# Performance work log

Measured on AMD Instinct MI355X. Metric: run time of the kernel, lower is better.

Reference implementation:

```python
import jax, jax.numpy as jnp
import numpy as np

B, S, H = 2, 1024, 4096
NH, NKV, HD = 32, 8, 128
GROUPS = NH // NKV  # num_key_value_groups
ROPE_THETA = 10000.0


def setup_inputs() -> dict:
    key = jax.random.key(0)
    k0, k1, k2 = jax.random.split(key, 3)
    x = jax.random.normal(k0, (B, S, H), jnp.float32)
    w_qkv = jax.random.normal(k1, (H, (NH + 2 * NKV) * HD), jnp.float32) * (1.0 / np.sqrt(H))
    w_o = jax.random.normal(k2, (NH * HD, H), jnp.float32) * (1.0 / np.sqrt(H))
    # rotary cos/sin tables (llama freqs_cis, interleaved-pair convention)
    inv_freq = 1.0 / (ROPE_THETA ** (np.arange(0, HD, 2, dtype=np.float64) / HD))
    freqs = np.outer(np.arange(S, dtype=np.float64), inv_freq)  # [S, HD/2]
    cos = jnp.asarray(np.cos(freqs), jnp.float32)
    sin = jnp.asarray(np.sin(freqs), jnp.float32)
    # additive causal mask [1,1,S,S]
    causal = np.tril(np.ones((S, S), dtype=bool))
    mask = jnp.asarray(np.where(causal, 0.0, -1e9), jnp.float32)[None, None]
    return {"x": x, "w_qkv": w_qkv, "w_o": w_o, "cos": cos, "sin": sin, "mask": mask}


def _rope(t, cos, sin):
    # t: [B,S,N,HD]; rotate interleaved (even, odd) pairs like complex mult by freqs_cis
    t2 = t.reshape(t.shape[:-1] + (HD // 2, 2))
    t0, t1 = t2[..., 0], t2[..., 1]
    c = cos[None, :, None, :]  # [1,S,1,HD/2]
    s = sin[None, :, None, :]
    r0 = t0 * c - t1 * s
    r1 = t0 * s + t1 * c
    return jnp.stack([r0, r1], axis=-1).reshape(t.shape)


def reference(x, w_qkv, w_o, cos, sin, mask):
    b, s, _ = x.shape
    xqkv = (x @ w_qkv).reshape(b, s, NH + 2 * NKV, HD)
    xq = xqkv[:, :, :NH]                  # [b,s,NH,HD]
    xk = xqkv[:, :, NH:NH + NKV]          # [b,s,NKV,HD]
    xv = xqkv[:, :, NH + NKV:]            # [b,s,NKV,HD]
    xq = _rope(xq, cos, sin)
    xk = _rope(xk, cos, sin)
    # GQA: repeat kv heads to match query heads (repeat_interleave on head dim)
    k = jnp.repeat(xk, GROUPS, axis=2)
    v = jnp.repeat(xv, GROUPS, axis=2)
    scores = jnp.einsum('bqhd,bkhd->bhqk', xq, k) / np.float32(np.sqrt(HD))
    scores = scores + mask
    probs = jax.nn.softmax(scores.astype(jnp.float32), axis=-1).astype(xq.dtype)
    out = jnp.einsum('bhqk,bkhd->bqhd', probs, v).reshape(b, s, NH * HD)
    return out @ w_o
```

## Files before the change

kernel.cpp:

```cpp
#include <hip/hip_runtime.h>
#include <cstdint>
#include <cstddef>

typedef short bf16x8 __attribute__((ext_vector_type(8)));
typedef float f32x4 __attribute__((ext_vector_type(4)));

__device__ __forceinline__ unsigned short f2bf(float f) {
  unsigned int u = __builtin_bit_cast(unsigned int, f);
  u += 0x7fffu + ((u >> 16) & 1u);
  return (unsigned short)(u >> 16);
}

__device__ __forceinline__ void transpose_tile(const float* __restrict__ src,
                                               unsigned short* __restrict__ dst,
                                               int K, int N, int n0, int k0, int tid) {
  __shared__ float t[64][65];
  const int lr = tid >> 4, lc = (tid & 15) * 4;
#pragma unroll
  for (int i = 0; i < 4; ++i) {
    float4 v = *(const float4*)(src + (size_t)(k0 + i * 16 + lr) * N + n0 + lc);
    t[i * 16 + lr][lc] = v.x;
    t[i * 16 + lr][lc + 1] = v.y;
    t[i * 16 + lr][lc + 2] = v.z;
    t[i * 16 + lr][lc + 3] = v.w;
  }
  __syncthreads();
  const int nr = tid >> 3, kk = (tid & 7) * 8;
#pragma unroll
  for (int i = 0; i < 2; ++i) {
    int n = nr + i * 32;
    bf16x8 v;
#pragma unroll
    for (int j = 0; j < 8; ++j) v[j] = (short)f2bf(t[kk + j][n]);
    *(bf16x8*)(dst + (size_t)(n0 + n) * K + k0 + kk) = v;
  }
}

__global__ __launch_bounds__(256) void k_prep(const float* __restrict__ x,
                                              const float* __restrict__ w_qkv,
                                              const float* __restrict__ w_o,
                                              unsigned short* __restrict__ xb,
                                              unsigned short* __restrict__ wqkv_t,
                                              unsigned short* __restrict__ wo_t) {
  const int bid = blockIdx.x, tid = threadIdx.x;
  if (bid < 8192) {
    int i = bid * 256 + tid;
    float4 v = ((const float4*)x)[i];
    ushort4 o;
    o.x = f2bf(v.x); o.y = f2bf(v.y); o.z = f2bf(v.z); o.w = f2bf(v.w);
    ((ushort4*)xb)[i] = o;
  } else if (bid < 14336) {
    int t = bid - 8192;
    transpose_tile(w_qkv, wqkv_t, 4096, 6144, (t % 96) * 64, (t / 96) * 64, tid);
  } else {
    int t = bid - 14336;
    transpose_tile(w_o, wo_t, 4096, 4096, (t & 63) * 64, (t >> 6) * 64, tid);
  }
}

template <int MODE>
__global__ __launch_bounds__(256) void k_gemm(const unsigned short* __restrict__ A,
                                              const unsigned short* __restrict__ Bt,
                                              float* __restrict__ C,
                                              unsigned short* __restrict__ Qr,
                                              unsigned short* __restrict__ Kr,
                                              unsigned short* __restrict__ Vt,
                                              const float* __restrict__ cosT,
                                              const float* __restrict__ sinT,
                                              int M, int N, int K) {
  __shared__ __align__(16) unsigned short lA[128 * 64];
  __shared__ __align__(16) unsigned short lB[128 * 64];
  const int tid = threadIdx.x;
  const int lane = tid & 63, wv = tid >> 6;
  const int wr = wv >> 1, wc = wv & 1;
  const int lid = blockIdx.y * gridDim.x + blockIdx.x;
  const int cpx = (gridDim.x * gridDim.y) >> 3;
  const int swz = (lid & 7) * cpx + (lid >> 3);
  const int bm = (swz % gridDim.x) * 128, bn = (swz / gridDim.x) * 128;
  const int l16 = lane & 15, lhi = lane >> 4;
  f32x4 acc[4][4] = {};
  bf16x8 ar[4], br[4];

#pragma unroll
  for (int i = 0; i < 4; ++i) {
    int c = tid + i * 256, row = c >> 3, c16 = c & 7;
    ar[i] = *(const bf16x8*)(A + (size_t)(bm + row) * K + 0 + c16 * 8);
    br[i] = *(const bf16x8*)(Bt + (size_t)(bn + row) * K + 0 + c16 * 8);
  }
  const int nkt = K >> 6;
  for (int kt = 0; kt < nkt; ++kt) {
    __syncthreads();
#pragma unroll
    for (int i = 0; i < 4; ++i) {
      int c = tid + i * 256, row = c >> 3, c16 = c & 7;
      int pc = c16 ^ (row & 7);
      *(bf16x8*)((char*)lA + row * 128 + pc * 16) = ar[i];
      *(bf16x8*)((char*)lB + row * 128 + pc * 16) = br[i];
    }
    __syncthreads();
    if (kt + 1 < nkt) {
      int kofs = (kt + 1) << 6;
#pragma unroll
      for (int i = 0; i < 4; ++i) {
        int c = tid + i * 256, row = c >> 3, c16 = c & 7;
        ar[i] = *(const bf16x8*)(A + (size_t)(bm + row) * K + kofs + c16 * 8);
        br[i] = *(const bf16x8*)(Bt + (size_t)(bn + row) * K + kofs + c16 * 8);
      }
    }
#pragma unroll
    for (int s = 0; s < 2; ++s) {
      bf16x8 af[4], bfr[4];
#pragma unroll
      for (int f = 0; f < 4; ++f) {
        int rowa = wr * 64 + f * 16 + l16;
        int ca = (s * 4 + lhi) ^ (rowa & 7);
        af[f] = *(const bf16x8*)((char*)lA + rowa * 128 + ca * 16);
        int rowb = wc * 64 + f * 16 + l16;
        int cb = (s * 4 + lhi) ^ (rowb & 7);
        bfr[f] = *(const bf16x8*)((char*)lB + rowb * 128 + cb * 16);
      }
#pragma unroll
      for (int fi = 0; fi < 4; ++fi)
#pragma unroll
        for (int fj = 0; fj < 4; ++fj)
          acc[fi][fj] = __builtin_amdgcn_mfma_f32_16x16x32_bf16(af[fi], bfr[fj], acc[fi][fj], 0, 0, 0);
    }
  }

  if (MODE == 0) {
#pragma unroll
    for (int fi = 0; fi < 4; ++fi) {
      int rbase = bm + wr * 64 + fi * 16 + lhi * 4;
#pragma unroll
      for (int fj = 0; fj < 4; ++fj) {
        int col = bn + wc * 64 + fj * 16 + l16;
#pragma unroll
        for (int r = 0; r < 4; ++r)
          C[(size_t)(rbase + r) * N + col] = acc[fi][fj][r];
      }
    }
  } else {
#pragma unroll
    for (int fi = 0; fi < 4; ++fi) {
      int rbase = bm + wr * 64 + fi * 16 + lhi * 4;
      int b = rbase >> 10, sbase = rbase & 1023;
#pragma unroll
      for (int fj = 0; fj < 4; ++fj) {
        int col = bn + wc * 64 + fj * 16 + l16;
        if (col < 5120) {
          int i = (col & 127) >> 1;
          float sgn = (col & 1) ? 1.0f : -1.0f;
          unsigned short* dst;
          if (col < 4096)
            dst = Qr + ((size_t)(b * 32 + (col >> 7)) * 1024) * 128 + (col & 127);
          else
            dst = Kr + ((size_t)(b * 8 + ((col - 4096) >> 7)) * 1024) * 128 + (col & 127);
#pragma unroll
          for (int r = 0; r < 4; ++r) {
            float own = acc[fi][fj][r];
            float other = __shfl_xor(own, 1);
            int s = sbase + r;
            float c = cosT[s * 64 + i], sn = sinT[s * 64 + i];
            dst[(size_t)s * 128] = f2bf(own * c + sgn * other * sn);
          }
        } else {
          int kvh = (col - 5120) >> 7, d = col & 127;
          unsigned short* dst = Vt + ((size_t)(b * 8 + kvh) * 128 + d) * 1024;
#pragma unroll
          for (int r = 0; r < 4; ++r) dst[sbase + r] = f2bf(acc[fi][fj][r]);
        }
      }
    }
  }
}

__global__ __launch_bounds__(256) void k_attn(const unsigned short* __restrict__ Qr,
                                              const unsigned short* __restrict__ Kr,
                                              const unsigned short* __restrict__ Vt,
                                              unsigned short* __restrict__ Out) {
  __shared__ __align__(16) unsigned short lK[64 * 128];
  __shared__ __align__(16) unsigned short lV[128 * 64];
  __shared__ __align__(16) unsigned short lP[4 * 16 * 64];
  const int tid = threadIdx.x, lane = tid & 63, wv = tid >> 6;
  const int qt = (int)gridDim.x - 1 - (int)blockIdx.x;
  const int h = blockIdx.y, b = blockIdx.z;
  const int kvh = h >> 2;
  const int q0 = qt * 64;
  const int l16 = lane & 15, lhi = lane >> 4;

  const unsigned short* Qbase = Qr + ((size_t)(b * 32 + h) * 1024 + q0 + wv * 16 + l16) * 128;
  bf16x8 qf[4];
#pragma unroll
  for (int s = 0; s < 4; ++s) qf[s] = *(const bf16x8*)(Qbase + s * 32 + lhi * 8);

  const unsigned short* Kbase = Kr + (size_t)(b * 8 + kvh) * 1024 * 128;
  const unsigned short* Vbase = Vt + (size_t)(b * 8 + kvh) * 128 * 1024;

  f32x4 oacc[8] = {};
  float mrow[4] = {-1e30f, -1e30f, -1e30f, -1e30f};
  float lrow[4] = {0.f, 0.f, 0.f, 0.f};
  const int ntk = qt + 1;
  bf16x8 kreg[4], vreg[4];

#pragma unroll
  for (int i = 0; i < 4; ++i) {
    int c = tid + i * 256;
    int krow = c >> 4, kc = c & 15;
    kreg[i] = *(const bf16x8*)(Kbase + (size_t)krow * 128 + kc * 8);
    int vrow = c >> 3, vc = c & 7;
    vreg[i] = *(const bf16x8*)(Vbase + (size_t)vrow * 1024 + vc * 8);
  }

  for (int kt = 0; kt < ntk; ++kt) {
    const int k0 = kt * 64;
    __syncthreads();
#pragma unroll
    for (int i = 0; i < 4; ++i) {
      int c = tid + i * 256;
      int krow = c >> 4, kc = c & 15;
      *(bf16x8*)((char*)lK + krow * 256 + (kc ^ (krow & 7)) * 16) = kreg[i];
      int vrow = c >> 3, vc = c & 7;
      *(bf16x8*)((char*)lV + vrow * 128 + (vc ^ (vrow & 7)) * 16) = vreg[i];
    }
    __syncthreads();

    if (kt + 1 < ntk) {
      const int kn = (kt + 1) * 64;
#pragma unroll
      for (int i = 0; i < 4; ++i) {
        int c = tid + i * 256;
        int krow = c >> 4, kc = c & 15;
        kreg[i] = *(const bf16x8*)(Kbase + (size_t)(kn + krow) * 128 + kc * 8);
        int vrow = c >> 3, vc = c & 7;
        vreg[i] = *(const bf16x8*)(Vbase + (size_t)vrow * 1024 + kn + vc * 8);
      }
    }

    f32x4 sacc[4] = {};
#pragma unroll
    for (int kf = 0; kf < 4; ++kf) {
      int rowk = kf * 16 + l16;
#pragma unroll
      for (int s = 0; s < 4; ++s) {
        int ck = (s * 4 + lhi) ^ (rowk & 7);
        bf16x8 kfr = *(const bf16x8*)((char*)lK + rowk * 256 + ck * 16);
        sacc[kf] = __builtin_amdgcn_mfma_f32_16x16x32_bf16(qf[s], kfr, sacc[kf], 0, 0, 0);
      }
    }

    const int qg = q0 + wv * 16 + lhi * 4;
    float mt[4] = {-1e30f, -1e30f, -1e30f, -1e30f};
#pragma unroll
    for (int kf = 0; kf < 4; ++kf) {
      int kg = k0 + kf * 16 + l16;
#pragma unroll
      for (int r = 0; r < 4; ++r) {
        float v = sacc[kf][r] * 0.08838834764831845f;
        v = (kg <= qg + r) ? v : -1e9f;
        sacc[kf][r] = v;
        mt[r] = fmaxf(mt[r], v);
      }
    }
#pragma unroll
    for (int r = 0; r < 4; ++r) {
#pragma unroll
      for (int off = 1; off < 16; off <<= 1) mt[r] = fmaxf(mt[r], __shfl_xor(mt[r], off));
    }

    bool need = false;
#pragma unroll
    for (int r = 0; r < 4; ++r) need = need || (mt[r] > mrow[r] + 8.0f);
    const bool doresc = (__ballot(need) != 0ull);

    float alpha[4], rs[4];
#pragma unroll
    for (int r = 0; r < 4; ++r) {
      if (doresc) {
        float mn = fmaxf(mrow[r], mt[r]);
        alpha[r] = __expf(mrow[r] - mn);
        mrow[r] = mn;
      } else {
        alpha[r] = 1.0f;
      }
      rs[r] = 0.f;
    }
#pragma unroll
    for (int kf = 0; kf < 4; ++kf) {
      int key = kf * 16 + l16;
#pragma unroll
      for (int r = 0; r < 4; ++r) {
        float p = __expf(sacc[kf][r] - mrow[r]);
        rs[r] += p;
        int prow = lhi * 4 + r;
        int addr = wv * 2048 + ((prow * 128 + key * 2) ^ ((prow & 7) << 4));
        *(unsigned short*)((char*)lP + addr) = f2bf(p);
      }
    }
#pragma unroll
    for (int r = 0; r < 4; ++r) {
#pragma unroll
      for (int off = 1; off < 16; off <<= 1) rs[r] += __shfl_xor(rs[r], off);
      lrow[r] = lrow[r] * alpha[r] + rs[r];
    }
    if (doresc) {
#pragma unroll
      for (int nf = 0; nf < 8; ++nf)
#pragma unroll
        for (int r = 0; r < 4; ++r) oacc[nf][r] *= alpha[r];
    }

#pragma unroll
    for (int s2 = 0; s2 < 2; ++s2) {
      int prow = l16;
      int paddr = wv * 2048 + ((prow * 128 + s2 * 64 + lhi * 16) ^ ((prow & 7) << 4));
      bf16x8 pa = *(const bf16x8*)((char*)lP + paddr);
#pragma unroll
      for (int nf = 0; nf < 8; ++nf) {
        int rowd = nf * 16 + l16;
        int cv = (s2 * 4 + lhi) ^ (rowd & 7);
        bf16x8 vfr = *(const bf16x8*)((char*)lV + rowd * 128 + cv * 16);
        oacc[nf] = __builtin_amdgcn_mfma_f32_16x16x32_bf16(pa, vfr, oacc[nf], 0, 0, 0);
      }
    }
  }

  unsigned short* Ob = Out + ((size_t)(b * 1024) + q0 + wv * 16 + lhi * 4) * 4096 + h * 128;
#pragma unroll
  for (int r = 0; r < 4; ++r) {
    float inv = 1.f / lrow[r];
#pragma unroll
    for (int nf = 0; nf < 8; ++nf)
      Ob[(size_t)r * 4096 + nf * 16 + l16] = f2bf(oacc[nf][r] * inv);
  }
}

extern "C" void kernel_launch(void* const* d_in, const int* in_sizes, int n_in,
                              void* d_out, int out_size, void* d_ws, size_t ws_size,
                              hipStream_t stream) {
  const float* x = (const float*)d_in[0];
  const float* w_qkv = (const float*)d_in[1];
  const float* w_o = (const float*)d_in[2];
  const float* cosT = (const float*)d_in[3];
  const float* sinT = (const float*)d_in[4];

  char* ws = (char*)d_ws;
  unsigned short* wqkv_t = (unsigned short*)(ws);
  unsigned short* wo_t   = (unsigned short*)(ws + 50331648);
  unsigned short* xb     = (unsigned short*)(ws + 83886080);
  unsigned short* Qr     = (unsigned short*)(ws + 100663296);
  unsigned short* Kr     = (unsigned short*)(ws + 117440512);
  unsigned short* Vt     = (unsigned short*)(ws + 121634816);
  unsigned short* attn   = (unsigned short*)(ws + 125829120);

  k_prep<<<18432, 256, 0, stream>>>(x, w_qkv, w_o, xb, wqkv_t, wo_t);
  k_gemm<1><<<dim3(16, 48), 256, 0, stream>>>(xb, wqkv_t, nullptr, Qr, Kr, Vt, cosT, sinT,
                                              2048, 6144, 4096);
  k_attn<<<dim3(16, 32, 2), 256, 0, stream>>>(Qr, Kr, Vt, attn);
  k_gemm<0><<<dim3(16, 32), 256, 0, stream>>>(attn, wo_t, (float*)d_out, nullptr, nullptr, nullptr,
                                              nullptr, nullptr, 2048, 4096, 4096);
}
```

Baseline: 325.3 us.

## Move w_o transpose into attention launch to overlap with attention blocks

The w_o fp32-to-bf16 transpose moves out of the prep kernel and into the attention kernel as 4096 extra blocks appended after the 1024 attention blocks. Those blocks run alongside the causal attention, whose blocks have uneven work, so the transpose can fill idle CUs and the prep kernel gets shorter. The attention kernel now uses a single shared buffer of 40 KB that both roles share, which may reduce occupancy for the transpose blocks compared with their own smaller allocation.

Measured after the change: 319.9 us. About the same (-1.7%).

```diff
diff --git a/kernel.cpp b/kernel.cpp
--- a/kernel.cpp
+++ b/kernel.cpp
@@ -13,16 +13,16 @@
 
 __device__ __forceinline__ void transpose_tile(const float* __restrict__ src,
                                                unsigned short* __restrict__ dst,
-                                               int K, int N, int n0, int k0, int tid) {
-  __shared__ float t[64][65];
-  const int lr = tid >> 4, lc = (tid & 15) * 4;
+                                               int K, int N, int n0, int k0, int tid,
+                                               float* __restrict__ tb ) {
 #pragma unroll
   for (int i = 0; i < 4; ++i) {
+    const int lr = tid >> 4, lc = (tid & 15) * 4;
     float4 v = *(const float4*)(src + (size_t)(k0 + i * 16 + lr) * N + n0 + lc);
-    t[i * 16 + lr][lc] = v.x;
-    t[i * 16 + lr][lc + 1] = v.y;
-    t[i * 16 + lr][lc + 2] = v.z;
-    t[i * 16 + lr][lc + 3] = v.w;
+    tb[(i * 16 + lr) * 65 + lc] = v.x;
+    tb[(i * 16 + lr) * 65 + lc + 1] = v.y;
+    tb[(i * 16 + lr) * 65 + lc + 2] = v.z;
+    tb[(i * 16 + lr) * 65 + lc + 3] = v.w;
   }
   __syncthreads();
   const int nr = tid >> 3, kk = (tid & 7) * 8;
@@ -31,17 +31,16 @@
     int n = nr + i * 32;
     bf16x8 v;
 #pragma unroll
-    for (int j = 0; j < 8; ++j) v[j] = (short)f2bf(t[kk + j][n]);
+    for (int j = 0; j < 8; ++j) v[j] = (short)f2bf(tb[(kk + j) * 65 + n]);
     *(bf16x8*)(dst + (size_t)(n0 + n) * K + k0 + kk) = v;
   }
 }
 
 __global__ __launch_bounds__(256) void k_prep(const float* __restrict__ x,
                                               const float* __restrict__ w_qkv,
-                                              const float* __restrict__ w_o,
                                               unsigned short* __restrict__ xb,
-                                              unsigned short* __restrict__ wqkv_t,
-                                              unsigned short* __restrict__ wo_t) {
+                                              unsigned short* __restrict__ wqkv_t) {
+  __shared__ float tb[64 * 65];
   const int bid = blockIdx.x, tid = threadIdx.x;
   if (bid < 8192) {
     int i = bid * 256 + tid;
@@ -49,12 +48,9 @@
     ushort4 o;
     o.x = f2bf(v.x); o.y = f2bf(v.y); o.z = f2bf(v.z); o.w = f2bf(v.w);
     ((ushort4*)xb)[i] = o;
-  } else if (bid < 14336) {
+  } else {
     int t = bid - 8192;
-    transpose_tile(w_qkv, wqkv_t, 4096, 6144, (t % 96) * 64, (t / 96) * 64, tid);
-  } else {
-    int t = bid - 14336;
-    transpose_tile(w_o, wo_t, 4096, 4096, (t & 63) * 64, (t >> 6) * 64, tid);
+    transpose_tile(w_qkv, wqkv_t, 4096, 6144, (t % 96) * 64, (t / 96) * 64, tid, tb);
   }
 }
 
@@ -174,16 +170,27 @@
   }
 }
 
-__global__ __launch_bounds__(256) void k_attn(const unsigned short* __restrict__ Qr,
-                                              const unsigned short* __restrict__ Kr,
-                                              const unsigned short* __restrict__ Vt,
-                                              unsigned short* __restrict__ Out) {
-  __shared__ __align__(16) unsigned short lK[64 * 128];
-  __shared__ __align__(16) unsigned short lV[128 * 64];
-  __shared__ __align__(16) unsigned short lP[4 * 16 * 64];
-  const int tid = threadIdx.x, lane = tid & 63, wv = tid >> 6;
-  const int qt = (int)gridDim.x - 1 - (int)blockIdx.x;
-  const int h = blockIdx.y, b = blockIdx.z;
+__global__ __launch_bounds__(256) void k_attn_wo(const unsigned short* __restrict__ Qr,
+                                                 const unsigned short* __restrict__ Kr,
+                                                 const unsigned short* __restrict__ Vt,
+                                                 unsigned short* __restrict__ Out,
+                                                 const float* __restrict__ w_o,
+                                                 unsigned short* __restrict__ wo_t) {
+  __shared__ __align__(16) char smem[40960];
+  const int bid = blockIdx.x, tid = threadIdx.x;
+
+  if (bid >= 1024) {
+    int t = bid - 1024;
+    transpose_tile(w_o, wo_t, 4096, 4096, (t & 63) * 64, (t >> 6) * 64, tid, (float*)smem);
+    return;
+  }
+
+  unsigned short* lK = (unsigned short*)smem;
+  unsigned short* lV = (unsigned short*)(smem + 16384);
+  unsigned short* lP = (unsigned short*)(smem + 32768);
+  const int lane = tid & 63, wv = tid >> 6;
+  const int qt = 15 - (bid & 15);
+  const int h = (bid >> 4) & 31, b = bid >> 9;
   const int kvh = h >> 2;
   const int q0 = qt * 64;
   const int l16 = lane & 15, lhi = lane >> 4;
@@ -352,10 +359,10 @@
   unsigned short* Vt     = (unsigned short*)(ws + 121634816);
   unsigned short* attn   = (unsigned short*)(ws + 125829120);
 
-  k_prep<<<18432, 256, 0, stream>>>(x, w_qkv, w_o, xb, wqkv_t, wo_t);
+  k_prep<<<14336, 256, 0, stream>>>(x, w_qkv, xb, wqkv_t);
   k_gemm<1><<<dim3(16, 48), 256, 0, stream>>>(xb, wqkv_t, nullptr, Qr, Kr, Vt, cosT, sinT,
                                               2048, 6144, 4096);
-  k_attn<<<dim3(16, 32, 2), 256, 0, stream>>>(Qr, Kr, Vt, attn);
+  k_attn_wo<<<1024 + 4096, 256, 0, stream>>>(Qr, Kr, Vt, attn, w_o, wo_t);
   k_gemm<0><<<dim3(16, 32), 256, 0, stream>>>(attn, wo_t, (float*)d_out, nullptr, nullptr, nullptr,
                                               nullptr, nullptr, 2048, 4096, 4096);
 }
```
